# Performance work log

Hardware: AMD Instinct MI355X
Metric: run time of the kernel (lower is better)

## Reference

```python
import jax, jax.numpy as jnp
import numpy as np

B, P, E, D, T = 16, 100, 5, 128, 4   # batch, patches, embedding levels, vector_dim, timesteps
G = 10                                # attention conv groups = sqrt(P)
HID = 32                              # CNN hidden channels
CG = P // G


def setup_inputs() -> dict:
    key = jax.random.key(0)
    ks = jax.random.split(key, 12)
    s = 0.005
    return {
        "x": jax.random.normal(ks[0], (B, 1, 28, 28), jnp.float32),
        "cnn_w": jax.random.normal(ks[1], (HID, 1, 3, 3), jnp.float32) * 0.1,
        "cnn_b": jnp.zeros((HID,), jnp.float32),
        "fc_w": jax.random.normal(ks[2], (D, HID), jnp.float32) * 0.1,
        "fc_b": jnp.zeros((D,), jnp.float32),
        "td_w": jax.random.normal(ks[3], (P * D, P * D + P), jnp.float32) * s,
        "td_b": jnp.zeros((P * D,), jnp.float32),
        "bu_w": jax.random.normal(ks[4], (P * D, P * D), jnp.float32) * s,
        "bu_b": jnp.zeros((P * D,), jnp.float32),
        "qw": jax.random.normal(ks[5], (G, CG, CG), jnp.float32) * 0.1,
        "qb": jnp.zeros((P,), jnp.float32),
        "kw": jax.random.normal(ks[6], (G, CG, CG), jnp.float32) * 0.1,
        "kb": jnp.zeros((P,), jnp.float32),
        "vw": jax.random.normal(ks[7], (G, CG, CG), jnp.float32) * 0.1,
        "vb": jnp.zeros((P,), jnp.float32),
        "gamma": jnp.ones((), jnp.float32),
    }


def reference(x, cnn_w, cnn_b, fc_w, fc_b, td_w, td_b, bu_w, bu_b,
              qw, qb, kw, kb, vw, vb, gamma):
    Bx = x.shape[0]
    # pad (1,1,1,1) -> (B,1,30,30), then non-overlapping 3x3 patches, row-major
    xp = jnp.pad(x, ((0, 0), (0, 0), (1, 1), (1, 1)))
    patches = (xp.reshape(Bx, 1, 10, 3, 10, 3)
                 .transpose(0, 2, 4, 1, 3, 5)
                 .reshape(Bx, P, 1, 3, 3))
    # CNN: 3x3 valid conv + relu + fc -> (B, P, D)
    h = jax.nn.relu(jnp.einsum('bpcij,ocij->bpo', patches, cnn_w) + cnn_b)
    emb = h @ fc_w.T + fc_b
    columns = jnp.broadcast_to(emb[:, :, None, :], (Bx, P, E, D))  # (B,P,E,D)
    pos = jnp.broadcast_to(jnp.arange(P, dtype=x.dtype), (Bx, P))

    def gconv(w, b, z):  # grouped 1x1 conv over channels P; z: (B,P,S)
        zg = z.reshape(Bx, G, CG, -1)
        return jnp.einsum('bgcs,goc->bgos', zg, w).reshape(Bx, P, -1) + b[None, :, None]

    def attend(t1):  # SAGAN-style self-attention over spatial axis (S = D); t1: (B,P,D)
        q = gconv(qw, qb, t1)
        k = gconv(kw, kb, t1)
        v = gconv(vw, vb, t1)
        a = jax.nn.softmax(jnp.einsum('bcn,bcm->bnm', q, k), axis=-1)  # (B,S,S)
        o = jnp.einsum('bcm,bnm->bcn', v, a)
        return gamma * o + t1

    def top_down(level):  # level: (B,P,D); input = flat level + position indices
        inp = jnp.concatenate([level.reshape(Bx, P * D), pos], axis=1)
        return (inp @ td_w.T + td_b).reshape(Bx, P, D)

    def bottom_up(level):
        return (level.reshape(Bx, P * D) @ bu_w.T + bu_b).reshape(Bx, P, D)

    def step(cols, _):
        new = []
        for i in range(E):
            t1 = cols[:, :, i, :]
            ta = attend(t1)
            if i == 0:
                c = t1 + 0.33 * top_down(cols[:, :, i + 1, :]) + 0.33 * ta
            elif i == E - 1:
                c = t1 + 0.33 * bottom_up(cols[:, :, i - 1, :]) + 0.33 * ta
            else:
                c = (t1 + 0.33 * top_down(cols[:, :, i + 1, :])
                     + 0.33 * bottom_up(cols[:, :, i - 1, :]) + 0.33 * ta)
            new.append(c)
        return jnp.stack(new, axis=2), None

    columns, _ = jax.lax.scan(step, columns, None, length=T - 1)
    return columns[:, :, E - 1, :].mean(axis=1)  # (B, D)
```

## Files before the change

### kernel.cpp

```cpp
#include <hip/hip_runtime.h>

#define BB 16
#define PP 100
#define EE 5
#define DD 128
#define GG 10
#define PD 12800
#define KTD 12900
#define BPD (BB*PD)

typedef __attribute__((ext_vector_type(4))) float f32x4;
typedef __attribute__((ext_vector_type(8))) short short8;
typedef __attribute__((ext_vector_type(4))) short short4v;

static __device__ __forceinline__ short f2bf(float f) {
  unsigned u = __builtin_bit_cast(unsigned, f);
  u += 0x7FFFu + ((u >> 16) & 1u);
  return (short)(u >> 16);
}

static __device__ __forceinline__ short8 cvt8(float4 a, float4 b) {
  short8 r;
  r[0] = f2bf(a.x); r[1] = f2bf(a.y); r[2] = f2bf(a.z); r[3] = f2bf(a.w);
  r[4] = f2bf(b.x); r[5] = f2bf(b.y); r[6] = f2bf(b.z); r[7] = f2bf(b.w);
  return r;
}

static __device__ __forceinline__ void gload16(const void* g, void* l) {
  __builtin_amdgcn_global_load_lds((const __attribute__((address_space(1))) void*)g,
                                   (__attribute__((address_space(3))) void*)l, 16, 0, 0);
}
static __device__ __forceinline__ void gload4(const void* g, void* l) {
  __builtin_amdgcn_global_load_lds((const __attribute__((address_space(1))) void*)g,
                                   (__attribute__((address_space(3))) void*)l, 4, 0, 0);
}

__global__ __launch_bounds__(128) void k_encoder(
    const float* __restrict__ x, const float* __restrict__ cw, const float* __restrict__ cb,
    const float* __restrict__ fw, const float* __restrict__ fb, float* __restrict__ cols) {
  int bid = blockIdx.x;
  int b = bid / 100, p = bid % 100;
  int py = p / 10, px = p % 10;
  __shared__ float patch[9];
  __shared__ float h[32];
  int tid = threadIdx.x;
  if (tid < 9) {
    int ii = tid / 3, jj = tid % 3;
    int gr = py * 3 + ii - 1, gc = px * 3 + jj - 1;
    float v = 0.f;
    if (gr >= 0 && gr < 28 && gc >= 0 && gc < 28) v = x[b * 784 + gr * 28 + gc];
    patch[tid] = v;
  }
  __syncthreads();
  if (tid < 32) {
    float a = cb[tid];
#pragma unroll
    for (int t = 0; t < 9; ++t) a += patch[t] * cw[tid * 9 + t];
    h[tid] = fmaxf(a, 0.f);
  }
  __syncthreads();
  float e = fb[tid];
#pragma unroll
  for (int o = 0; o < 32; ++o) e += h[o] * fw[tid * 32 + o];
  long bp = (long)b * PP + p;
  for (int lev = 0; lev < EE; ++lev)
    cols[((long)lev * BB * PP + bp) * DD + tid] = e;
}

__global__ __launch_bounds__(256) void k_tdbias(
    const float* __restrict__ td_w, const float* __restrict__ td_b, float* __restrict__ out) {
  int o = blockIdx.x * 256 + threadIdx.x;
  if (o >= PD) return;
  float s = td_b[o];
  const float4* r = (const float4*)(td_w + (long)o * KTD + PD);
#pragma unroll
  for (int q = 0; q < 25; ++q) {
    float4 v = r[q];
    float p0 = (float)(q * 4);
    s += p0 * v.x + (p0 + 1.f) * v.y + (p0 + 2.f) * v.z + (p0 + 3.f) * v.w;
  }
  out[o] = s;
}

#define MSTRIDE (1600L * 16 * 8)

__global__ __launch_bounds__(256) void k_packa(
    const float* __restrict__ src, short* __restrict__ dst) {
  int bid = blockIdx.x;
  int rb = bid / 8;
  int kc = bid % 8;
  int t = threadIdx.x;
  int r = t >> 4, c = t & 15;
  long srow = ((long)rb * 16 + r) * PD;
  for (int kk = 0; kk < 25; ++kk) {
    int k = kc * 1600 + kk * 64 + c * 4;
    float4 v = *(const float4*)(src + srow + k);
    short4v o;
    o[0] = f2bf(v.x); o[1] = f2bf(v.y); o[2] = f2bf(v.z); o[3] = f2bf(v.w);
    long di = (((long)rb * 1600 + (k >> 3)) * 16 + r) * 8 + (k & 7);
    *(short4v*)(dst + di) = o;
  }
}

__global__ __launch_bounds__(256) void k_gemm_f(
    const float* __restrict__ td_w, const float* __restrict__ bu_w,
    const short* __restrict__ Ap, short* __restrict__ wtd, short* __restrict__ wbu,
    float* __restrict__ ytd, float* __restrict__ ybu) {
  int bid = blockIdx.x;
  int which = bid / 800;
  int r = bid % 800;
  int kc = r / 200;
  int nb = r % 200;
  int w = threadIdx.x >> 6;
  int lane = threadIdx.x & 63;
  int l15 = lane & 15, l4 = lane >> 4;
  const float* W = which ? bu_w : td_w;
  long ldw = which ? PD : KTD;
  short* WP = which ? wbu : wtd;
  float* Y = which ? ybu : ytd;
  int lev0 = which ? 0 : 1;
  int nb16 = nb * 4 + w;
  __shared__ float lBf[2][4096];
  __shared__ short lA[2][4096];
  const float* bsrc[16];
#pragma unroll
  for (int c = 0; c < 16; ++c)
    bsrc[c] = W + (long)(nb16 * 16 + c) * ldw + kc * 3200 + (lane ^ ((c & 7) * 8));
  const short* sA = Ap + (long)(lev0 + w) * MSTRIDE + (long)kc * 51200 + lane * 8;
  short* wp = WP + (long)nb16 * MSTRIDE + (((long)kc * 400 + l4) * 16 + l15) * 8;
  int lbase = w * 1024;
#define STAGE_F(bufi) { \
  float* bdst = lBf[bufi]; short* adst = lA[bufi]; \
  _Pragma("unroll") \
  for (int c = 0; c < 16; ++c) gload4(bsrc[c], bdst + lbase + c * 64); \
  gload16(sA, adst + lbase); \
  gload16(sA + 512, adst + lbase + 512); \
  _Pragma("unroll") \
  for (int c = 0; c < 16; ++c) bsrc[c] += 64; \
  sA += 1024; }
  STAGE_F(0)
  f32x4 acc0 = {0,0,0,0}, acc1 = {0,0,0,0}, acc2 = {0,0,0,0}, acc3 = {0,0,0,0};
  int bswz = (l15 & 7) * 8;
  for (int s = 0; s < 50; ++s) {
    __syncthreads();
    int cur = s & 1;
    if (s < 49) STAGE_F(cur ^ 1)
#pragma unroll
    for (int ks = 0; ks < 2; ++ks) {
      int fb_ = lbase + l15 * 64 + ((ks * 32 + l4 * 8) ^ bswz);
      float4 b0 = *(const float4*)&lBf[cur][fb_];
      float4 b1 = *(const float4*)&lBf[cur][fb_ + 4];
      short8 bF = cvt8(b0, b1);
      *(short8*)(wp + (long)(s * 8 + ks * 4) * 128) = bF;
      int off = ks * 512 + l4 * 128 + l15 * 8;
      short8 a0 = *(const short8*)&lA[cur][0 * 1024 + off];
      short8 a1 = *(const short8*)&lA[cur][1 * 1024 + off];
      short8 a2 = *(const short8*)&lA[cur][2 * 1024 + off];
      short8 a3 = *(const short8*)&lA[cur][3 * 1024 + off];
      acc0 = __builtin_amdgcn_mfma_f32_16x16x32_bf16(a0, bF, acc0, 0, 0, 0);
      acc1 = __builtin_amdgcn_mfma_f32_16x16x32_bf16(a1, bF, acc1, 0, 0, 0);
      acc2 = __builtin_amdgcn_mfma_f32_16x16x32_bf16(a2, bF, acc2, 0, 0, 0);
      acc3 = __builtin_amdgcn_mfma_f32_16x16x32_bf16(a3, bF, acc3, 0, 0, 0);
    }
  }
#undef STAGE_F
  float* yb = Y + (long)kc * 64 * PD;
  int col = nb16 * 16 + l15;
#pragma unroll
  for (int j = 0; j < 4; ++j) yb[(long)(0 * 16 + l4 * 4 + j) * PD + col] = acc0[j];
#pragma unroll
  for (int j = 0; j < 4; ++j) yb[(long)(1 * 16 + l4 * 4 + j) * PD + col] = acc1[j];
#pragma unroll
  for (int j = 0; j < 4; ++j) yb[(long)(2 * 16 + l4 * 4 + j) * PD + col] = acc2[j];
#pragma unroll
  for (int j = 0; j < 4; ++j) yb[(long)(3 * 16 + l4 * 4 + j) * PD + col] = acc3[j];
}

__global__ __launch_bounds__(256) void k_gemm_p(
    const short* __restrict__ Ap, const short* __restrict__ wtd,
    const short* __restrict__ wbu, float* __restrict__ ytd, float* __restrict__ ybu) {
  int bid = blockIdx.x;
  int which = bid / 800;
  int r = bid % 800;
  int kc = r / 200;
  int nb = r % 200;
  int w = threadIdx.x >> 6;
  int lane = threadIdx.x & 63;
  int l15 = lane & 15, l4 = lane >> 4;
  const short* Wp = which ? wbu : wtd;
  float* Y = which ? ybu : ytd;
  int lev0 = which ? 0 : 1;
  int nb16 = nb * 4 + w;
  __shared__ short lA[2][4096];
  __shared__ short lB[2][4096];
  const short* sB = Wp + (long)nb16 * MSTRIDE + (long)kc * 51200 + lane * 8;
  const short* sA = Ap + (long)(lev0 + w) * MSTRIDE + (long)kc * 51200 + lane * 8;
  int lbase = w * 1024;
#define STAGE_G(bufi) { \
  gload16(sB,       &lB[bufi][lbase]); \
  gload16(sB + 512, &lB[bufi][lbase + 512]); \
  gload16(sA,       &lA[bufi][lbase]); \
  gload16(sA + 512, &lA[bufi][lbase + 512]); \
  sB += 1024; sA += 1024; }
  STAGE_G(0)
  f32x4 acc0 = {0,0,0,0}, acc1 = {0,0,0,0}, acc2 = {0,0,0,0}, acc3 = {0,0,0,0};
  int fo = l4 * 128 + l15 * 8;
  for (int s = 0; s < 50; ++s) {
    __syncthreads();
    int cur = s & 1;
    if (s < 49) STAGE_G(cur ^ 1)
#pragma unroll
    for (int ks = 0; ks < 2; ++ks) {
      int off = ks * 512 + fo;
      short8 bF = *(const short8*)&lB[cur][w * 1024 + off];
      short8 a0 = *(const short8*)&lA[cur][0 * 1024 + off];
      short8 a1 = *(const short8*)&lA[cur][1 * 1024 + off];
      short8 a2 = *(const short8*)&lA[cur][2 * 1024 + off];
      short8 a3 = *(const short8*)&lA[cur][3 * 1024 + off];
      acc0 = __builtin_amdgcn_mfma_f32_16x16x32_bf16(a0, bF, acc0, 0, 0, 0);
      acc1 = __builtin_amdgcn_mfma_f32_16x16x32_bf16(a1, bF, acc1, 0, 0, 0);
      acc2 = __builtin_amdgcn_mfma_f32_16x16x32_bf16(a2, bF, acc2, 0, 0, 0);
      acc3 = __builtin_amdgcn_mfma_f32_16x16x32_bf16(a3, bF, acc3, 0, 0, 0);
    }
  }
#undef STAGE_G
  float* yb = Y + (long)kc * 64 * PD;
  int col = nb16 * 16 + l15;
#pragma unroll
  for (int j = 0; j < 4; ++j) yb[(long)(0 * 16 + l4 * 4 + j) * PD + col] = acc0[j];
#pragma unroll
  for (int j = 0; j < 4; ++j) yb[(long)(1 * 16 + l4 * 4 + j) * PD + col] = acc1[j];
#pragma unroll
  for (int j = 0; j < 4; ++j) yb[(long)(2 * 16 + l4 * 4 + j) * PD + col] = acc2[j];
#pragma unroll
  for (int j = 0; j < 4; ++j) yb[(long)(3 * 16 + l4 * 4 + j) * PD + col] = acc3[j];
}

__global__ __launch_bounds__(256) void k_gemm(
    const float* __restrict__ cols, const float* __restrict__ td_w,
    const float* __restrict__ bu_w, float* __restrict__ ytd, float* __restrict__ ybu) {
  int bid = blockIdx.x;
  int which = bid / 800;
  int r = bid % 800;
  int kc = r / 200;
  int nb = r % 200;
  const float* X; const float* W; long ldw; float* Y;
  if (which == 0) { X = cols + BPD; W = td_w; ldw = KTD; Y = ytd; }
  else            { X = cols;       W = bu_w; ldw = PD;  Y = ybu; }
  int wave = threadIdx.x >> 6;
  int lane = threadIdx.x & 63;
  int l15 = lane & 15, l4 = lane >> 4;
  int n0 = nb * 64 + wave * 16;
  int k0 = kc * 3200 + l4 * 8;
  const float* ap = X + (long)l15 * PD + k0;
  const float* bp = W + (long)(n0 + l15) * ldw + k0;
  f32x4 acc[4] = {{0,0,0,0},{0,0,0,0},{0,0,0,0},{0,0,0,0}};
  for (int kk = 0; kk < 100; ++kk) {
    float4 b0 = *(const float4*)bp;
    float4 b1 = *(const float4*)(bp + 4);
    short8 bf = cvt8(b0, b1);
#pragma unroll
    for (int m = 0; m < 4; ++m) {
      const float* a_ = ap + (long)m * 16 * PD;
      float4 a0 = *(const float4*)a_;
      float4 a1 = *(const float4*)(a_ + 4);
      short8 af = cvt8(a0, a1);
      acc[m] = __builtin_amdgcn_mfma_f32_16x16x32_bf16(af, bf, acc[m], 0, 0, 0);
    }
    ap += 32; bp += 32;
  }
  float* yb = Y + (long)kc * 64 * PD;
  int col = n0 + l15;
#pragma unroll
  for (int m = 0; m < 4; ++m)
#pragma unroll
    for (int j = 0; j < 4; ++j)
      yb[(long)(m * 16 + l4 * 4 + j) * PD + col] = acc[m][j];
}

__global__ __launch_bounds__(256) void k_att(
    const float* __restrict__ cols,
    const float* __restrict__ qw, const float* __restrict__ qb,
    const float* __restrict__ kw, const float* __restrict__ kb,
    const float* __restrict__ vw, const float* __restrict__ vb,
    const float* __restrict__ ytd, const float* __restrict__ ybu,
    const float* __restrict__ tdbias, const float* __restrict__ bub,
    const float* __restrict__ gamma,
    float* __restrict__ colsn, short* __restrict__ apack, int emit) {
  __shared__ float smem[38400];
  float* T1 = smem;
  float* V  = smem + 12800;
  float* OL = smem + 25600;
  float* QG = smem + 25600;
  float* KG = smem + 26880;
  float* WB = smem + 28160;
  int ib = blockIdx.x;
  int i = ib >> 4, b = ib & 15;
  int t = threadIdx.x;
  const float* t1b = cols + (long)ib * PD;
  for (int idx = t; idx < PD; idx += 256) T1[idx] = t1b[idx];
  for (int idx = t; idx < 300; idx += 256) {
    int w3 = idx / 100, c = idx % 100;
    WB[idx] = (w3 == 0 ? qw[c] : w3 == 1 ? kw[c] : vw[c]);
  }
  __syncthreads();
  int s = t & 127, oh = t >> 7;
  int mq = t & 3, nh = t >> 2;
  float acc0[32], acc1[32];
#pragma unroll
  for (int j = 0; j < 32; ++j) { acc0[j] = 0.f; acc1[j] = 0.f; }
  for (int g = 0; g < 10; ++g) {
    float aq[5], ak[5], av[5];
#pragma unroll
    for (int r = 0; r < 5; ++r) {
      int p = g * 10 + r * 2 + oh;
      aq[r] = qb[p]; ak[r] = kb[p]; av[r] = vb[p];
    }
    for (int c = 0; c < 10; ++c) {
      float z = T1[(g * 10 + c) * 128 + s];
#pragma unroll
      for (int r = 0; r < 5; ++r) {
        int o = r * 2 + oh;
        aq[r] += WB[o * 10 + c] * z;
        ak[r] += WB[100 + o * 10 + c] * z;
        av[r] += WB[200 + o * 10 + c] * z;
      }
    }
    __syncthreads();
#pragma unroll
    for (int r = 0; r < 5; ++r) {
      int o = r * 2 + oh;
      QG[o * 128 + s] = aq[r];
      KG[o * 128 + s] = ak[r];
      V[(g * 10 + o) * 128 + s] = av[r];
    }
    if (g < 9) {
      for (int idx = t; idx < 300; idx += 256) {
        int w3 = idx / 100, c = idx % 100;
        int gi = (g + 1) * 100 + c;
        WB[idx] = (w3 == 0 ? qw[gi] : w3 == 1 ? kw[gi] : vw[gi]);
      }
    }
    __syncthreads();
    const float4* K4 = (const float4*)KG;
    for (int c = 0; c < 10; ++c) {
      float qa = QG[c * 128 + nh];
      float qc = QG[c * 128 + nh + 64];
#pragma unroll
      for (int jj = 0; jj < 8; ++jj) {
        float4 kv = K4[c * 32 + mq * 8 + jj];
        acc0[jj * 4 + 0] += qa * kv.x; acc0[jj * 4 + 1] += qa * kv.y;
        acc0[jj * 4 + 2] += qa * kv.z; acc0[jj * 4 + 3] += qa * kv.w;
        acc1[jj * 4 + 0] += qc * kv.x; acc1[jj * 4 + 1] += qc * kv.y;
        acc1[jj * 4 + 2] += qc * kv.z; acc1[jj * 4 + 3] += qc * kv.w;
      }
    }
    __syncthreads();
  }
  {
    float mx = acc0[0];
#pragma unroll
    for (int j = 1; j < 32; ++j) mx = fmaxf(mx, acc0[j]);
    mx = fmaxf(mx, __shfl_xor(mx, 1)); mx = fmaxf(mx, __shfl_xor(mx, 2));
    float sm = 0.f;
#pragma unroll
    for (int j = 0; j < 32; ++j) { acc0[j] = __expf(acc0[j] - mx); sm += acc0[j]; }
    sm += __shfl_xor(sm, 1); sm += __shfl_xor(sm, 2);
    float inv = 1.0f / sm;
#pragma unroll
    for (int j = 0; j < 32; ++j) acc0[j] *= inv;
  }
  {
    float mx = acc1[0];
#pragma unroll
    for (int j = 1; j < 32; ++j) mx = fmaxf(mx, acc1[j]);
    mx = fmaxf(mx, __shfl_xor(mx, 1)); mx = fmaxf(mx, __shfl_xor(mx, 2));
    float sm = 0.f;
#pragma unroll
    for (int j = 0; j < 32; ++j) { acc1[j] = __expf(acc1[j] - mx); sm += acc1[j]; }
    sm += __shfl_xor(sm, 1); sm += __shfl_xor(sm, 2);
    float inv = 1.0f / sm;
#pragma unroll
    for (int j = 0; j < 32; ++j) acc1[j] *= inv;
  }
  const float4* V4 = (const float4*)V;
  for (int p = 0; p < 100; ++p) {
    float pa = 0.f, pb = 0.f;
#pragma unroll
    for (int jj = 0; jj < 8; ++jj) {
      float4 vv = V4[p * 32 + mq * 8 + jj];
      pa += acc0[jj * 4 + 0] * vv.x + acc0[jj * 4 + 1] * vv.y
          + acc0[jj * 4 + 2] * vv.z + acc0[jj * 4 + 3] * vv.w;
      pb += acc1[jj * 4 + 0] * vv.x + acc1[jj * 4 + 1] * vv.y
          + acc1[jj * 4 + 2] * vv.z + acc1[jj * 4 + 3] * vv.w;
    }
    pa += __shfl_xor(pa, 1); pa += __shfl_xor(pa, 2);
    pb += __shfl_xor(pb, 1); pb += __shfl_xor(pb, 2);
    if ((p & 3) == mq) {
      OL[p * 128 + nh] = pa;
      OL[p * 128 + nh + 64] = pb;
    }
  }
  __syncthreads();
  float gam = gamma[0];
  bool has_td = (i < EE - 1);
  bool has_bu = (i > 0);
  const float* ytdr = ytd + ((long)i * BB + b) * PD;
  const float* ybur = ybu + ((long)(i - 1) * BB + b) * PD;
  const long CH = 64L * PD;
  float* outb = colsn + (long)ib * PD;
  short* ap_ = apack;
  for (int od = t; od < PD; od += 256) {
    float t1 = T1[od];
    float ov = OL[od];
    float accv = t1 + 0.33f * (gam * ov + t1);
    if (has_td) {
      float y = tdbias[od] + ytdr[od] + ytdr[CH + od] + ytdr[2 * CH + od] + ytdr[3 * CH + od];
      accv += 0.33f * y;
    }
    if (has_bu) {
      float y = bub[od] + ybur[od] + ybur[CH + od] + ybur[2 * CH + od] + ybur[3 * CH + od];
      accv += 0.33f * y;
    }
    outb[od] = accv;
    if (emit)
      ap_[(((long)i * 1600 + (od >> 3)) * 16 + b) * 8 + (od & 7)] = f2bf(accv);
  }
}

__global__ __launch_bounds__(128) void k_mean(const float* __restrict__ cols, float* __restrict__ out) {
  int b = blockIdx.x, d = threadIdx.x;
  const float* base = cols + ((long)4 * BB + b) * PP * DD + d;
  float s0 = 0.f, s1 = 0.f, s2 = 0.f, s3 = 0.f;
  for (int p = 0; p < 100; p += 4) {
    s0 += base[(long)p * DD];
    s1 += base[(long)(p + 1) * DD];
    s2 += base[(long)(p + 2) * DD];
    s3 += base[(long)(p + 3) * DD];
  }
  out[b * DD + d] = (s0 + s1 + s2 + s3) / 100.0f;
}

extern "C" void kernel_launch(void* const* d_in, const int* in_sizes, int n_in,
                              void* d_out, int out_size, void* d_ws, size_t ws_size,
                              hipStream_t stream) {
  const float* x     = (const float*)d_in[0];
  const float* cnn_w = (const float*)d_in[1];
  const float* cnn_b = (const float*)d_in[2];
  const float* fc_w  = (const float*)d_in[3];
  const float* fc_b  = (const float*)d_in[4];
  const float* td_w  = (const float*)d_in[5];
  const float* td_b  = (const float*)d_in[6];
  const float* bu_w  = (const float*)d_in[7];
  const float* bu_b  = (const float*)d_in[8];
  const float* qw    = (const float*)d_in[9];
  const float* qb    = (const float*)d_in[10];
  const float* kw    = (const float*)d_in[11];
  const float* kb    = (const float*)d_in[12];
  const float* vw    = (const float*)d_in[13];
  const float* vb    = (const float*)d_in[14];
  const float* gamma = (const float*)d_in[15];
  float* out = (float*)d_out;
  float* ws = (float*)d_ws;

  float* cols_a = ws;
  float* cols_b = ws + 1024000;
  float* ytd    = ws + 6430720;
  float* ybu    = ws + 9707520;
  float* tdbias = ws + 12984320;
  short* wtd_p  = (short*)(ws + 12997120);
  short* wbu_p  = wtd_p + 163840000;
  short* apack  = wbu_p + 163840000;
  size_t need_bytes = (size_t)12997120 * 4 + (163840000ULL * 2 + 1024000ULL + 8192ULL) * 2;
  bool packed = ws_size >= need_bytes;

  k_encoder<<<1600, 128, 0, stream>>>(x, cnn_w, cnn_b, fc_w, fc_b, cols_a);
  k_tdbias<<<50, 256, 0, stream>>>(td_w, td_b, tdbias);
  if (packed) k_packa<<<40, 256, 0, stream>>>(cols_a, apack);

  float* cur = cols_a;
  float* nxt = cols_b;
  for (int t = 0; t < 3; ++t) {
    if (packed) {
      if (t == 0)
        k_gemm_f<<<1600, 256, 0, stream>>>(td_w, bu_w, apack, wtd_p, wbu_p, ytd, ybu);
      else
        k_gemm_p<<<1600, 256, 0, stream>>>(apack, wtd_p, wbu_p, ytd, ybu);
    } else {
      k_gemm<<<1600, 256, 0, stream>>>(cur, td_w, bu_w, ytd, ybu);
    }
    int emit = (packed && t < 2) ? 1 : 0;
    k_att<<<80, 256, 0, stream>>>(cur, qw, qb, kw, kb, vw, vb,
                                  ytd, ybu, tdbias, bu_b, gamma, nxt, apack, emit);
    float* tmp = cur; cur = nxt; nxt = tmp;
  }
  k_mean<<<16, 128, 0, stream>>>(cur, out);
}
```

Baseline: 1.136 ms.

## Halve split-K factor and stage fp32 weights through registers in first GEMM

The split-K count for the top-down/bottom-up GEMMs drops from four to two, so each block covers twice the K range. This halves the partial-sum writes and the reads in the attention epilogue, at the cost of half as many blocks. The first-pass GEMM, which converts fp32 weights to packed bf16, now loads weight rows into registers with float4 loads. It then writes them to a larger swizzled LDS tile instead of using 4-byte global-to-LDS loads, and double-buffers A over bigger stages. The trade is fewer blocks and more LDS and registers for wider loads and less reduction traffic.

```diff
diff --git a/kernel.cpp b/kernel.cpp
--- a/kernel.cpp
+++ b/kernel.cpp
@@ -29,10 +29,6 @@
 static __device__ __forceinline__ void gload16(const void* g, void* l) {
   __builtin_amdgcn_global_load_lds((const __attribute__((address_space(1))) void*)g,
                                    (__attribute__((address_space(3))) void*)l, 16, 0, 0);
-}
-static __device__ __forceinline__ void gload4(const void* g, void* l) {
-  __builtin_amdgcn_global_load_lds((const __attribute__((address_space(1))) void*)g,
-                                   (__attribute__((address_space(3))) void*)l, 4, 0, 0);
 }
 
 __global__ __launch_bounds__(128) void k_encoder(
@@ -107,8 +103,8 @@
     const short* __restrict__ Ap, short* __restrict__ wtd, short* __restrict__ wbu,
     float* __restrict__ ytd, float* __restrict__ ybu) {
   int bid = blockIdx.x;
-  int which = bid / 800;
-  int r = bid % 800;
+  int which = bid / 400;
+  int r = bid % 400;
   int kc = r / 200;
   int nb = r % 200;
   int w = threadIdx.x >> 6;
@@ -120,50 +116,51 @@
   float* Y = which ? ybu : ytd;
   int lev0 = which ? 0 : 1;
   int nb16 = nb * 4 + w;
-  __shared__ float lBf[2][4096];
-  __shared__ short lA[2][4096];
-  const float* bsrc[16];
-#pragma unroll
-  for (int c = 0; c < 16; ++c)
-    bsrc[c] = W + (long)(nb16 * 16 + c) * ldw + kc * 3200 + (lane ^ ((c & 7) * 8));
-  const short* sA = Ap + (long)(lev0 + w) * MSTRIDE + (long)kc * 51200 + lane * 8;
-  short* wp = WP + (long)nb16 * MSTRIDE + (((long)kc * 400 + l4) * 16 + l15) * 8;
-  int lbase = w * 1024;
-#define STAGE_F(bufi) { \
-  float* bdst = lBf[bufi]; short* adst = lA[bufi]; \
-  _Pragma("unroll") \
-  for (int c = 0; c < 16; ++c) gload4(bsrc[c], bdst + lbase + c * 64); \
-  gload16(sA, adst + lbase); \
-  gload16(sA + 512, adst + lbase + 512); \
-  _Pragma("unroll") \
-  for (int c = 0; c < 16; ++c) bsrc[c] += 64; \
-  sA += 1024; }
-  STAGE_F(0)
+  __shared__ float lBf[64 * 256];
+  __shared__ short lA[2][4][4096];
+  const float* rp[16];
+#pragma unroll
+  for (int j = 0; j < 16; ++j)
+    rp[j] = W + (long)(nb16 * 16 + j) * ldw + kc * 6400
+          + (((lane >> 1) ^ (j & 7)) << 3) + ((lane & 1) << 2);
+  const short* sA = Ap + (long)(lev0 + w) * MSTRIDE + (long)kc * 102400 + lane * 8;
+  short* wp = WP + (long)nb16 * MSTRIDE + (long)kc * 102400;
+  float4 c[16];
+#define LOADB(ss) { _Pragma("unroll") \
+  for (int j = 0; j < 16; ++j) c[j] = *(const float4*)(rp[j] + (ss) * 256); }
+#define AGLOAD(buf, ss) { _Pragma("unroll") \
+  for (int i = 0; i < 8; ++i) gload16(sA + (ss) * 4096 + i * 512, &lA[buf][w][i * 512]); }
+  AGLOAD(0, 0)
+  LOADB(0)
   f32x4 acc0 = {0,0,0,0}, acc1 = {0,0,0,0}, acc2 = {0,0,0,0}, acc3 = {0,0,0,0};
-  int bswz = (l15 & 7) * 8;
-  for (int s = 0; s < 50; ++s) {
+  for (int ss = 0; ss < 25; ++ss) {
+    int cur = ss & 1;
+#pragma unroll
+    for (int j = 0; j < 16; ++j)
+      *(float4*)&lBf[(w * 16 + j) * 256 + lane * 4] = c[j];
     __syncthreads();
-    int cur = s & 1;
-    if (s < 49) STAGE_F(cur ^ 1)
-#pragma unroll
-    for (int ks = 0; ks < 2; ++ks) {
-      int fb_ = lbase + l15 * 64 + ((ks * 32 + l4 * 8) ^ bswz);
-      float4 b0 = *(const float4*)&lBf[cur][fb_];
-      float4 b1 = *(const float4*)&lBf[cur][fb_ + 4];
+    if (ss < 24) { AGLOAD(cur ^ 1, ss + 1) LOADB(ss + 1) }
+#pragma unroll
+    for (int t = 0; t < 8; ++t) {
+      int u = (t * 4 + l4) ^ (l15 & 7);
+      const float* bp_ = &lBf[(w * 16 + l15) * 256 + u * 8];
+      float4 b0 = *(const float4*)bp_;
+      float4 b1 = *(const float4*)(bp_ + 4);
       short8 bF = cvt8(b0, b1);
-      *(short8*)(wp + (long)(s * 8 + ks * 4) * 128) = bF;
-      int off = ks * 512 + l4 * 128 + l15 * 8;
-      short8 a0 = *(const short8*)&lA[cur][0 * 1024 + off];
-      short8 a1 = *(const short8*)&lA[cur][1 * 1024 + off];
-      short8 a2 = *(const short8*)&lA[cur][2 * 1024 + off];
-      short8 a3 = *(const short8*)&lA[cur][3 * 1024 + off];
+      *(short8*)(wp + ((long)(ss * 32 + t * 4 + l4) * 16 + l15) * 8) = bF;
+      int off = ((t * 4 + l4) * 16 + l15) * 8;
+      short8 a0 = *(const short8*)&lA[cur][0][off];
+      short8 a1 = *(const short8*)&lA[cur][1][off];
+      short8 a2 = *(const short8*)&lA[cur][2][off];
+      short8 a3 = *(const short8*)&lA[cur][3][off];
       acc0 = __builtin_amdgcn_mfma_f32_16x16x32_bf16(a0, bF, acc0, 0, 0, 0);
       acc1 = __builtin_amdgcn_mfma_f32_16x16x32_bf16(a1, bF, acc1, 0, 0, 0);
       acc2 = __builtin_amdgcn_mfma_f32_16x16x32_bf16(a2, bF, acc2, 0, 0, 0);
       acc3 = __builtin_amdgcn_mfma_f32_16x16x32_bf16(a3, bF, acc3, 0, 0, 0);
     }
   }
-#undef STAGE_F
+#undef LOADB
+#undef AGLOAD
   float* yb = Y + (long)kc * 64 * PD;
   int col = nb16 * 16 + l15;
 #pragma unroll
@@ -180,8 +177,8 @@
     const short* __restrict__ Ap, const short* __restrict__ wtd,
     const short* __restrict__ wbu, float* __restrict__ ytd, float* __restrict__ ybu) {
   int bid = blockIdx.x;
-  int which = bid / 800;
-  int r = bid % 800;
+  int which = bid / 400;
+  int r = bid % 400;
   int kc = r / 200;
   int nb = r % 200;
   int w = threadIdx.x >> 6;
@@ -193,8 +190,8 @@
   int nb16 = nb * 4 + w;
   __shared__ short lA[2][4096];
   __shared__ short lB[2][4096];
-  const short* sB = Wp + (long)nb16 * MSTRIDE + (long)kc * 51200 + lane * 8;
-  const short* sA = Ap + (long)(lev0 + w) * MSTRIDE + (long)kc * 51200 + lane * 8;
+  const short* sB = Wp + (long)nb16 * MSTRIDE + (long)kc * 102400 + lane * 8;
+  const short* sA = Ap + (long)(lev0 + w) * MSTRIDE + (long)kc * 102400 + lane * 8;
   int lbase = w * 1024;
 #define STAGE_G(bufi) { \
   gload16(sB,       &lB[bufi][lbase]); \
@@ -205,10 +202,10 @@
   STAGE_G(0)
   f32x4 acc0 = {0,0,0,0}, acc1 = {0,0,0,0}, acc2 = {0,0,0,0}, acc3 = {0,0,0,0};
   int fo = l4 * 128 + l15 * 8;
-  for (int s = 0; s < 50; ++s) {
+  for (int s = 0; s < 100; ++s) {
     __syncthreads();
     int cur = s & 1;
-    if (s < 49) STAGE_G(cur ^ 1)
+    if (s < 99) STAGE_G(cur ^ 1)
 #pragma unroll
     for (int ks = 0; ks < 2; ++ks) {
       int off = ks * 512 + fo;
@@ -240,8 +237,8 @@
     const float* __restrict__ cols, const float* __restrict__ td_w,
     const float* __restrict__ bu_w, float* __restrict__ ytd, float* __restrict__ ybu) {
   int bid = blockIdx.x;
-  int which = bid / 800;
-  int r = bid % 800;
+  int which = bid / 400;
+  int r = bid % 400;
   int kc = r / 200;
   int nb = r % 200;
   const float* X; const float* W; long ldw; float* Y;
@@ -251,11 +248,11 @@
   int lane = threadIdx.x & 63;
   int l15 = lane & 15, l4 = lane >> 4;
   int n0 = nb * 64 + wave * 16;
-  int k0 = kc * 3200 + l4 * 8;
+  int k0 = kc * 6400 + l4 * 8;
   const float* ap = X + (long)l15 * PD + k0;
   const float* bp = W + (long)(n0 + l15) * ldw + k0;
   f32x4 acc[4] = {{0,0,0,0},{0,0,0,0},{0,0,0,0},{0,0,0,0}};
-  for (int kk = 0; kk < 100; ++kk) {
+  for (int kk = 0; kk < 200; ++kk) {
     float4 b0 = *(const float4*)bp;
     float4 b1 = *(const float4*)(bp + 4);
     short8 bf = cvt8(b0, b1);
@@ -415,11 +412,11 @@
     float ov = OL[od];
     float accv = t1 + 0.33f * (gam * ov + t1);
     if (has_td) {
-      float y = tdbias[od] + ytdr[od] + ytdr[CH + od] + ytdr[2 * CH + od] + ytdr[3 * CH + od];
+      float y = tdbias[od] + ytdr[od] + ytdr[CH + od];
       accv += 0.33f * y;
     }
     if (has_bu) {
-      float y = bub[od] + ybur[od] + ybur[CH + od] + ybur[2 * CH + od] + ybur[3 * CH + od];
+      float y = bub[od] + ybur[od] + ybur[CH + od];
       accv += 0.33f * y;
     }
     outb[od] = accv;
@@ -483,11 +480,11 @@
   for (int t = 0; t < 3; ++t) {
     if (packed) {
       if (t == 0)
-        k_gemm_f<<<1600, 256, 0, stream>>>(td_w, bu_w, apack, wtd_p, wbu_p, ytd, ybu);
+        k_gemm_f<<<800, 256, 0, stream>>>(td_w, bu_w, apack, wtd_p, wbu_p, ytd, ybu);
       else
-        k_gemm_p<<<1600, 256, 0, stream>>>(apack, wtd_p, wbu_p, ytd, ybu);
+        k_gemm_p<<<800, 256, 0, stream>>>(apack, wtd_p, wbu_p, ytd, ybu);
     } else {
-      k_gemm<<<1600, 256, 0, stream>>>(cur, td_w, bu_w, ytd, ybu);
+      k_gemm<<<800, 256, 0, stream>>>(cur, td_w, bu_w, ytd, ybu);
     }
     int emit = (packed && t < 2) ? 1 : 0;
     k_att<<<80, 256, 0, stream>>>(cur, qw, qb, kw, kb, vw, vb,
```

New measurement: 1.459 ms. +28.4%, slower.
